# Performance work log

Measured on AMD Instinct MI355X. Metric: run time of the kernel, lower is better.

## Reference

```python
import jax, jax.numpy as jnp
import numpy as np

E = 8          # num_experts
K = 2          # top_k
TEMP = 1.0     # router_temp
D = 1024       # model dim
H = 4 * D      # expert hidden dim
B, T = 2, 2048


def setup_inputs() -> dict:
    key = jax.random.key(0)
    ks = jax.random.split(key, 5)
    x = jax.random.normal(ks[0], (B, T, D), jnp.float32)
    gate_w = jax.random.normal(ks[1], (D, E), jnp.float32) * 0.02
    gate_b = jnp.zeros((E,), jnp.float32)
    w1 = jax.random.normal(ks[2], (E, D, H), jnp.float32) * 0.02
    b1 = jnp.zeros((E, H), jnp.float32)
    w2 = jax.random.normal(ks[3], (E, H, D), jnp.float32) * 0.02
    b2 = jnp.zeros((E, D), jnp.float32)
    return {"x": x, "gate_w": gate_w, "gate_b": gate_b,
            "w1": w1, "b1": b1, "w2": w2, "b2": b2}


def reference(x, gate_w, gate_b, w1, b1, w2, b2):
    b, t, d = x.shape
    xf = x.reshape(-1, d)                                    # [N, D]
    logits = xf @ gate_w + gate_b                            # [N, E]
    gates = jax.nn.softmax(logits / TEMP, axis=-1)
    topk_gates, topk_idx = jax.lax.top_k(gates, K)           # [N, K]
    topk_gates = topk_gates / (topk_gates.sum(-1, keepdims=True) + 1e-9)
    # combine weight per (token, expert): sum over k slots routed to expert e
    comb = (jax.nn.one_hot(topk_idx, E, dtype=xf.dtype)
            * topk_gates[..., None]).sum(axis=1)             # [N, E]
    out = jnp.zeros_like(xf)
    for e in range(E):  # small fixed loop over experts
        h = jax.nn.gelu(xf @ w1[e] + b1[e], approximate=False)  # exact GELU (torch default)
        out = out + comb[:, e:e + 1] * (h @ w2[e] + b2[e])
    return out.reshape(b, t, d)
```

## Files before the change

kernel.cpp:

```cpp
#include <hip/hip_runtime.h>
#include <math.h>

#define NTOK 4096
#define DIM  1024
#define HID  4096
#define NEXP 8
#define NROW 8192

typedef __bf16 bf16;
typedef __attribute__((ext_vector_type(8))) __bf16 bf16x8;
typedef __attribute__((ext_vector_type(4))) float floatx4;

__device__ __forceinline__ void gl_lds16(const bf16* g, bf16* l) {
    __builtin_amdgcn_global_load_lds(
        (const __attribute__((address_space(1))) void*)g,
        (__attribute__((address_space(3))) void*)l, 16, 0, 0);
}

__global__ void zero_k(int* __restrict__ p) {
    if (threadIdx.x < 16) p[threadIdx.x] = 0;
}

__global__ __launch_bounds__(256) void convx_k(const float* __restrict__ x,
                                               bf16* __restrict__ xb)
{
    size_t gid = (size_t)blockIdx.x * 256 + threadIdx.x;
    size_t eo = gid * 8;
    floatx4 a = *(const floatx4*)(x + eo);
    floatx4 b = *(const floatx4*)(x + eo + 4);
    bf16x8 v;
#pragma unroll
    for (int j = 0; j < 4; ++j) { v[j] = (bf16)a[j]; v[4 + j] = (bf16)b[j]; }
    *(bf16x8*)&xb[eo] = v;
}

__global__ __launch_bounds__(256) void router_k(
    const float* __restrict__ x, const float* __restrict__ gw, const float* __restrict__ gb,
    int* __restrict__ counts, int* __restrict__ tok_e, float* __restrict__ tok_g)
{
    __shared__ __align__(16) float gws[DIM * NEXP];
    int t = threadIdx.x;
#pragma unroll
    for (int i = 0; i < 8; ++i)
        *(floatx4*)&gws[(t * 8 + i) * 4] = *(const floatx4*)&gw[(t * 8 + i) * 4];
    __syncthreads();

    int gid = blockIdx.x * 256 + t;
    int wv = gid >> 6, lane = gid & 63;
    const float* xr = x + (size_t)wv * DIM;
    float acc[NEXP];
#pragma unroll
    for (int e = 0; e < NEXP; ++e) acc[e] = 0.f;
    int d0 = lane * 16;
#pragma unroll
    for (int j = 0; j < 16; ++j) {
        float xv = xr[d0 + j];
#pragma unroll
        for (int e = 0; e < NEXP; ++e) acc[e] += xv * gws[(d0 + j) * NEXP + e];
    }
#pragma unroll
    for (int off = 32; off > 0; off >>= 1) {
#pragma unroll
        for (int e = 0; e < NEXP; ++e) acc[e] += __shfl_xor(acc[e], off, 64);
    }
    if (lane == 0) {
        float lg[NEXP], m = -1e30f;
        for (int e = 0; e < NEXP; ++e) { lg[e] = acc[e] + gb[e]; m = fmaxf(m, lg[e]); }
        float p[NEXP], s = 0.f;
        for (int e = 0; e < NEXP; ++e) { p[e] = expf(lg[e] - m); s += p[e]; }
        int e0 = 0;
        for (int e = 1; e < NEXP; ++e) if (p[e] > p[e0]) e0 = e;
        int e1 = (e0 == 0) ? 1 : 0;
        for (int e = 0; e < NEXP; ++e) if (e != e0 && p[e] > p[e1]) e1 = e;
        float g0 = p[e0] / s, g1 = p[e1] / s;
        float gs = g0 + g1 + 1e-9f;
        g0 /= gs; g1 /= gs;
        tok_e[wv * 2] = e0; tok_e[wv * 2 + 1] = e1;
        tok_g[wv * 2] = g0; tok_g[wv * 2 + 1] = g1;
        atomicAdd(&counts[e0], 1);
        atomicAdd(&counts[e1], 1);
    }
}

__global__ void scan_k(const int* __restrict__ counts, int* __restrict__ base)
{
    if (threadIdx.x == 0) {
        int s = 0;
#pragma unroll
        for (int e = 0; e < NEXP; ++e) { base[e] = s; s += counts[e]; }
        base[NEXP] = s;
    }
}

__global__ __launch_bounds__(256) void scatter_k(
    const int* __restrict__ tok_e, const float* __restrict__ tok_g,
    const int* __restrict__ base, int* __restrict__ counts2,
    int* __restrict__ row_token, float* __restrict__ row_gate, int* __restrict__ tok_row)
{
    int tk = blockIdx.x * 256 + threadIdx.x;
    if (tk >= NTOK) return;
#pragma unroll
    for (int k = 0; k < 2; ++k) {
        int e = tok_e[tk * 2 + k];
        int slot = atomicAdd(&counts2[e], 1);
        int r = base[e] + slot;
        row_token[r] = tk;
        row_gate[r] = tok_g[tk * 2 + k];
        tok_row[tk * 2 + k] = r;
    }
}

__global__ __launch_bounds__(256) void transpose_k(
    const float* __restrict__ src, bf16* __restrict__ dst,
    int R, int sld, size_t soff, size_t es, size_t ed)
{
    int e = blockIdx.z;
    bf16* d = dst + (size_t)e * ed;
    __shared__ __align__(16) bf16 tile[64 * 64];
    int t = threadIdx.x;
    int r0 = blockIdx.y * 64, c0 = blockIdx.x * 64;
#pragma unroll
    for (int i = 0; i < 2; ++i) {
        int c = t + i * 256;
        int rr = c >> 3, cc = c & 7;
        size_t eo = soff + (size_t)e * es + (size_t)(r0 + rr) * sld + c0 + cc * 8;
        floatx4 a = *(const floatx4*)(src + eo);
        floatx4 b = *(const floatx4*)(src + eo + 4);
        bf16x8 v;
#pragma unroll
        for (int j = 0; j < 4; ++j) { v[j] = (bf16)a[j]; v[4 + j] = (bf16)b[j]; }
        *(bf16x8*)&tile[rr * 64 + ((cc ^ ((rr >> 3) & 7)) * 8)] = v;
    }
    __syncthreads();
#pragma unroll
    for (int i = 0; i < 2; ++i) {
        int c = t + i * 256;
        int oc = c >> 3;
        int occ = c & 7;
        bf16x8 v;
#pragma unroll
        for (int j = 0; j < 8; ++j) {
            int r = occ * 8 + j;
            int p = (oc >> 3) ^ ((r >> 3) & 7);
            v[j] = tile[r * 64 + p * 8 + (oc & 7)];
        }
        *(bf16x8*)&d[(size_t)(c0 + oc) * R + r0 + occ * 8] = v;
    }
}

__global__ __launch_bounds__(256) void gemm1_k(
    const bf16* __restrict__ xb, const bf16* __restrict__ w1t, const float* __restrict__ b1,
    const int* __restrict__ counts, const int* __restrict__ base,
    const int* __restrict__ row_token, bf16* __restrict__ hbuf, int Nc, int bias_off)
{
    const int e = blockIdx.z;
    const int cnt = counts[e];
    const int rt = blockIdx.y;
    if (rt * 128 >= cnt) return;
    const int rb = base[e] + rt * 128;
    const int rend = base[e] + cnt;
    const int n0 = blockIdx.x * 128;

    __shared__ __align__(16) bf16 As[128 * 32];
    __shared__ __align__(16) bf16 Bs[128 * 32];

    const int t = threadIdx.x;
    const int wv = t >> 6, lane = t & 63;
    const int s0 = t, s1 = t + 256;
    const int ar0 = s0 >> 2, ac0 = (s0 & 3) ^ ((s0 >> 3) & 3);
    const int ar1 = s1 >> 2, ac1 = (s1 & 3) ^ ((s1 >> 3) & 3);
    int rr0 = rb + ar0; if (rr0 > NROW - 1) rr0 = NROW - 1;
    int rr1 = rb + ar1; if (rr1 > NROW - 1) rr1 = NROW - 1;
    const bf16* ga0 = xb + (size_t)row_token[rr0] * DIM + ac0 * 8;
    const bf16* ga1 = xb + (size_t)row_token[rr1] * DIM + ac1 * 8;
    const bf16* wb = w1t + (size_t)e * Nc * DIM;
    const bf16* gb0 = wb + (size_t)(n0 + ar0) * DIM + ac0 * 8;
    const bf16* gb1 = wb + (size_t)(n0 + ar1) * DIM + ac1 * 8;
    bf16* lA0 = &As[wv * 512];
    bf16* lA1 = &As[2048 + wv * 512];
    bf16* lB0 = &Bs[wv * 512];
    bf16* lB1 = &Bs[2048 + wv * 512];

    floatx4 acc[4][4];
#pragma unroll
    for (int i = 0; i < 4; ++i)
#pragma unroll
        for (int j = 0; j < 4; ++j) acc[i][j] = floatx4{0.f, 0.f, 0.f, 0.f};

    const int wr = (wv >> 1) * 64, wc = (wv & 1) * 64;
    const int lr = lane & 15;
    const int ck = lane >> 4;

    for (int k0 = 0; k0 < DIM; k0 += 32) {
        __syncthreads();
        gl_lds16(ga0 + k0, lA0);
        gl_lds16(ga1 + k0, lA1);
        gl_lds16(gb0 + k0, lB0);
        gl_lds16(gb1 + k0, lB1);
        __syncthreads();
        bf16x8 af[4], bg[4];
#pragma unroll
        for (int i = 0; i < 4; ++i) {
            int r = wr + i * 16 + lr;
            af[i] = *(const bf16x8*)&As[r * 32 + ((ck ^ ((r >> 1) & 3)) * 8)];
        }
#pragma unroll
        for (int i = 0; i < 4; ++i) {
            int r = wc + i * 16 + lr;
            bg[i] = *(const bf16x8*)&Bs[r * 32 + ((ck ^ ((r >> 1) & 3)) * 8)];
        }
#pragma unroll
        for (int mi = 0; mi < 4; ++mi)
#pragma unroll
            for (int ni = 0; ni < 4; ++ni)
                acc[mi][ni] = __builtin_amdgcn_mfma_f32_16x16x32_bf16(af[mi], bg[ni], acc[mi][ni], 0, 0, 0);
    }

#pragma unroll
    for (int mi = 0; mi < 4; ++mi) {
#pragma unroll
        for (int r = 0; r < 4; ++r) {
            int m = wr + mi * 16 + (lane >> 4) * 4 + r;
            int gr = rb + m;
            if (gr < rend) {
#pragma unroll
                for (int ni = 0; ni < 4; ++ni) {
                    int col = n0 + wc + ni * 16 + lr;
                    float v = acc[mi][ni][r] + b1[e * HID + bias_off + col];
                    v = 0.5f * v * (1.f + erff(v * 0.70710678f));
                    hbuf[(size_t)gr * Nc + col] = (bf16)v;
                }
            }
        }
    }
}

__global__ __launch_bounds__(256) void gemm2_k(
    const bf16* __restrict__ hbuf, const bf16* __restrict__ w2t, const float* __restrict__ b2,
    const int* __restrict__ counts, const int* __restrict__ base,
    const float* __restrict__ row_gate, float* __restrict__ ybuf,
    int Kc, int first, int last)
{
    const int e = blockIdx.z;
    const int cnt = counts[e];
    const int rt = blockIdx.y;
    if (rt * 128 >= cnt) return;
    const int rb = base[e] + rt * 128;
    const int rend = base[e] + cnt;
    const int n0 = blockIdx.x * 128;

    __shared__ __align__(16) bf16 As[128 * 32];
    __shared__ __align__(16) bf16 Bs[128 * 32];

    const int t = threadIdx.x;
    const int wv = t >> 6, lane = t & 63;
    const int s0 = t, s1 = t + 256;
    const int ar0 = s0 >> 2, ac0 = (s0 & 3) ^ ((s0 >> 3) & 3);
    const int ar1 = s1 >> 2, ac1 = (s1 & 3) ^ ((s1 >> 3) & 3);
    int rr0 = rb + ar0; if (rr0 > NROW - 1) rr0 = NROW - 1;
    int rr1 = rb + ar1; if (rr1 > NROW - 1) rr1 = NROW - 1;
    const bf16* ga0 = hbuf + (size_t)rr0 * Kc + ac0 * 8;
    const bf16* ga1 = hbuf + (size_t)rr1 * Kc + ac1 * 8;
    const bf16* wb = w2t + (size_t)e * DIM * Kc;
    const bf16* gb0 = wb + (size_t)(n0 + ar0) * Kc + ac0 * 8;
    const bf16* gb1 = wb + (size_t)(n0 + ar1) * Kc + ac1 * 8;
    bf16* lA0 = &As[wv * 512];
    bf16* lA1 = &As[2048 + wv * 512];
    bf16* lB0 = &Bs[wv * 512];
    bf16* lB1 = &Bs[2048 + wv * 512];

    floatx4 acc[4][4];
#pragma unroll
    for (int i = 0; i < 4; ++i)
#pragma unroll
        for (int j = 0; j < 4; ++j) acc[i][j] = floatx4{0.f, 0.f, 0.f, 0.f};

    const int wr = (wv >> 1) * 64, wc = (wv & 1) * 64;
    const int lr = lane & 15;
    const int ck = lane >> 4;

    for (int k0 = 0; k0 < Kc; k0 += 32) {
        __syncthreads();
        gl_lds16(ga0 + k0, lA0);
        gl_lds16(ga1 + k0, lA1);
        gl_lds16(gb0 + k0, lB0);
        gl_lds16(gb1 + k0, lB1);
        __syncthreads();
        bf16x8 af[4], bg[4];
#pragma unroll
        for (int i = 0; i < 4; ++i) {
            int r = wr + i * 16 + lr;
            af[i] = *(const bf16x8*)&As[r * 32 + ((ck ^ ((r >> 1) & 3)) * 8)];
        }
#pragma unroll
        for (int i = 0; i < 4; ++i) {
            int r = wc + i * 16 + lr;
            bg[i] = *(const bf16x8*)&Bs[r * 32 + ((ck ^ ((r >> 1) & 3)) * 8)];
        }
#pragma unroll
        for (int mi = 0; mi < 4; ++mi)
#pragma unroll
            for (int ni = 0; ni < 4; ++ni)
                acc[mi][ni] = __builtin_amdgcn_mfma_f32_16x16x32_bf16(af[mi], bg[ni], acc[mi][ni], 0, 0, 0);
    }

#pragma unroll
    for (int mi = 0; mi < 4; ++mi) {
#pragma unroll
        for (int r = 0; r < 4; ++r) {
            int m = wr + mi * 16 + (lane >> 4) * 4 + r;
            int gr = rb + m;
            if (gr < rend) {
#pragma unroll
                for (int ni = 0; ni < 4; ++ni) {
                    int col = n0 + wc + ni * 16 + lr;
                    size_t idx = (size_t)gr * DIM + col;
                    float v = acc[mi][ni][r];
                    if (last) {
                        float prev = first ? 0.f : ybuf[idx];
                        ybuf[idx] = row_gate[gr] * (prev + v + b2[e * DIM + col]);
                    } else {
                        ybuf[idx] = first ? v : (ybuf[idx] + v);
                    }
                }
            }
        }
    }
}

__global__ __launch_bounds__(256) void combine_k(
    const float* __restrict__ ybuf, const int* __restrict__ tok_row, float* __restrict__ out)
{
    int i = blockIdx.x * 256 + threadIdx.x;
    int tk = i >> 8;
    int dc = (i & 255) * 4;
    int ra = tok_row[tk * 2], rb = tok_row[tk * 2 + 1];
    floatx4 a = *(const floatx4*)&ybuf[(size_t)ra * DIM + dc];
    floatx4 b = *(const floatx4*)&ybuf[(size_t)rb * DIM + dc];
    floatx4 o;
#pragma unroll
    for (int j = 0; j < 4; ++j) o[j] = a[j] + b[j];
    *(floatx4*)&out[(size_t)tk * DIM + dc] = o;
}

extern "C" void kernel_launch(void* const* d_in, const int* in_sizes, int n_in,
                              void* d_out, int out_size, void* d_ws, size_t ws_size,
                              hipStream_t stream)
{
    const float* x  = (const float*)d_in[0];
    const float* gw = (const float*)d_in[1];
    const float* gb = (const float*)d_in[2];
    const float* w1 = (const float*)d_in[3];
    const float* b1 = (const float*)d_in[4];
    const float* w2 = (const float*)d_in[5];
    const float* b2 = (const float*)d_in[6];
    float* out = (float*)d_out;

    char* w = (char*)d_ws;
    int*   counts  = (int*)(w + 0);
    int*   counts2 = (int*)(w + 32);
    int*   base    = (int*)(w + 64);
    int*   tok_e   = (int*)(w + 256);
    float* tok_g   = (float*)(w + 256 + 32768);
    int*   row_tok = (int*)(w + 256 + 2 * 32768);
    float* row_g   = (float*)(w + 256 + 3 * 32768);
    int*   tok_row = (int*)(w + 256 + 4 * 32768);
    size_t off = 256 + 5 * 32768;
    bf16*  xb   = (bf16*)(w + off);   off += (size_t)NTOK * DIM * 2;
    float* ybuf = (float*)(w + off);  off += (size_t)NROW * DIM * 4;

    int Hc = HID;
    for (;;) {
        size_t need = off + (size_t)NEXP * Hc * DIM * 2 + (size_t)NROW * Hc * 2;
        if (need <= ws_size || Hc == 128) break;
        Hc >>= 1;
    }
    bf16* wT   = (bf16*)(w + off);  off += (size_t)NEXP * Hc * DIM * 2;
    bf16* hbuf = (bf16*)(w + off);

    zero_k<<<1, 64, 0, stream>>>(counts);
    router_k<<<NTOK / 4, 256, 0, stream>>>(x, gw, gb, counts, tok_e, tok_g);
    scan_k<<<1, 64, 0, stream>>>(counts, base);
    scatter_k<<<NTOK / 256, 256, 0, stream>>>(tok_e, tok_g, base, counts2, row_tok, row_g, tok_row);
    convx_k<<<(NTOK * DIM) / 2048, 256, 0, stream>>>(x, xb);

    const int nc = HID / Hc;
    for (int ch = 0; ch < nc; ++ch) {
        transpose_k<<<dim3(Hc / 64, DIM / 64, NEXP), 256, 0, stream>>>(
            w1, wT, DIM, HID, (size_t)ch * Hc, (size_t)DIM * HID, (size_t)Hc * DIM);
        gemm1_k<<<dim3(Hc / 128, 32, NEXP), 256, 0, stream>>>(
            xb, wT, b1, counts, base, row_tok, hbuf, Hc, ch * Hc);
        transpose_k<<<dim3(DIM / 64, Hc / 64, NEXP), 256, 0, stream>>>(
            w2, wT, Hc, DIM, (size_t)ch * Hc * DIM, (size_t)HID * DIM, (size_t)DIM * Hc);
        gemm2_k<<<dim3(DIM / 128, 32, NEXP), 256, 0, stream>>>(
            hbuf, wT, b2, counts, base, row_g, ybuf, Hc, ch == 0, ch == nc - 1);
    }

    combine_k<<<NTOK, 256, 0, stream>>>(ybuf, tok_row, out);
}
```

Baseline: 754.3 us.

## Double-buffer GEMM LDS loads and split-K gemm2 with atomic accumulation

Both expert GEMMs now prefetch the next K tile into a second LDS buffer while computing the current one, cutting one barrier per iteration. gemm2 is split four ways along K, with each slice atomically adding into a zeroed fp32 buffer to increase block-level parallelism. The gate scaling and b2 bias move into the combine kernel. This adds a zeroing pass and atomic traffic, and makes summation order nondeterministic.

After: 765.0 us. About the same (+1.4%).

```diff
diff --git a/kernel.cpp b/kernel.cpp
--- a/kernel.cpp
+++ b/kernel.cpp
@@ -6,6 +6,7 @@
 #define HID  4096
 #define NEXP 8
 #define NROW 8192
+#define KSPLIT 4
 
 typedef __bf16 bf16;
 typedef __attribute__((ext_vector_type(8))) __bf16 bf16x8;
@@ -19,6 +20,11 @@
 
 __global__ void zero_k(int* __restrict__ p) {
     if (threadIdx.x < 16) p[threadIdx.x] = 0;
+}
+
+__global__ __launch_bounds__(256) void zeroy_k(float* __restrict__ p) {
+    size_t i = ((size_t)blockIdx.x * 256 + threadIdx.x) * 4;
+    *(floatx4*)(p + i) = floatx4{0.f, 0.f, 0.f, 0.f};
 }
 
 __global__ __launch_bounds__(256) void convx_k(const float* __restrict__ x,
@@ -161,8 +167,8 @@
     const int rend = base[e] + cnt;
     const int n0 = blockIdx.x * 128;
 
-    __shared__ __align__(16) bf16 As[128 * 32];
-    __shared__ __align__(16) bf16 Bs[128 * 32];
+    __shared__ __align__(16) bf16 As[2][128 * 32];
+    __shared__ __align__(16) bf16 Bs[2][128 * 32];
 
     const int t = threadIdx.x;
     const int wv = t >> 6, lane = t & 63;
@@ -176,10 +182,7 @@
     const bf16* wb = w1t + (size_t)e * Nc * DIM;
     const bf16* gb0 = wb + (size_t)(n0 + ar0) * DIM + ac0 * 8;
     const bf16* gb1 = wb + (size_t)(n0 + ar1) * DIM + ac1 * 8;
-    bf16* lA0 = &As[wv * 512];
-    bf16* lA1 = &As[2048 + wv * 512];
-    bf16* lB0 = &Bs[wv * 512];
-    bf16* lB1 = &Bs[2048 + wv * 512];
+    const int off0 = wv * 512, off1 = 2048 + wv * 512;
 
     floatx4 acc[4][4];
 #pragma unroll
@@ -191,29 +194,39 @@
     const int lr = lane & 15;
     const int ck = lane >> 4;
 
+    gl_lds16(ga0, &As[0][off0]);
+    gl_lds16(ga1, &As[0][off1]);
+    gl_lds16(gb0, &Bs[0][off0]);
+    gl_lds16(gb1, &Bs[0][off1]);
+    __syncthreads();
+
+    int cur = 0;
     for (int k0 = 0; k0 < DIM; k0 += 32) {
-        __syncthreads();
-        gl_lds16(ga0 + k0, lA0);
-        gl_lds16(ga1 + k0, lA1);
-        gl_lds16(gb0 + k0, lB0);
-        gl_lds16(gb1 + k0, lB1);
-        __syncthreads();
+        const int kn = k0 + 32;
+        if (kn < DIM) {
+            gl_lds16(ga0 + kn, &As[cur ^ 1][off0]);
+            gl_lds16(ga1 + kn, &As[cur ^ 1][off1]);
+            gl_lds16(gb0 + kn, &Bs[cur ^ 1][off0]);
+            gl_lds16(gb1 + kn, &Bs[cur ^ 1][off1]);
+        }
         bf16x8 af[4], bg[4];
 #pragma unroll
         for (int i = 0; i < 4; ++i) {
             int r = wr + i * 16 + lr;
-            af[i] = *(const bf16x8*)&As[r * 32 + ((ck ^ ((r >> 1) & 3)) * 8)];
+            af[i] = *(const bf16x8*)&As[cur][r * 32 + ((ck ^ ((r >> 1) & 3)) * 8)];
         }
 #pragma unroll
         for (int i = 0; i < 4; ++i) {
             int r = wc + i * 16 + lr;
-            bg[i] = *(const bf16x8*)&Bs[r * 32 + ((ck ^ ((r >> 1) & 3)) * 8)];
+            bg[i] = *(const bf16x8*)&Bs[cur][r * 32 + ((ck ^ ((r >> 1) & 3)) * 8)];
         }
 #pragma unroll
         for (int mi = 0; mi < 4; ++mi)
 #pragma unroll
             for (int ni = 0; ni < 4; ++ni)
                 acc[mi][ni] = __builtin_amdgcn_mfma_f32_16x16x32_bf16(af[mi], bg[ni], acc[mi][ni], 0, 0, 0);
+        __syncthreads();
+        cur ^= 1;
     }
 
 #pragma unroll
@@ -236,21 +249,23 @@
 }
 
 __global__ __launch_bounds__(256) void gemm2_k(
-    const bf16* __restrict__ hbuf, const bf16* __restrict__ w2t, const float* __restrict__ b2,
+    const bf16* __restrict__ hbuf, const bf16* __restrict__ w2t,
     const int* __restrict__ counts, const int* __restrict__ base,
-    const float* __restrict__ row_gate, float* __restrict__ ybuf,
-    int Kc, int first, int last)
-{
-    const int e = blockIdx.z;
+    float* __restrict__ ybuf, int Kc)
+{
+    const int e  = blockIdx.z >> 2;
+    const int ks = blockIdx.z & 3;
     const int cnt = counts[e];
     const int rt = blockIdx.y;
     if (rt * 128 >= cnt) return;
     const int rb = base[e] + rt * 128;
     const int rend = base[e] + cnt;
     const int n0 = blockIdx.x * 128;
-
-    __shared__ __align__(16) bf16 As[128 * 32];
-    __shared__ __align__(16) bf16 Bs[128 * 32];
+    const int klen = Kc / KSPLIT;
+    const int kbeg = ks * klen;
+
+    __shared__ __align__(16) bf16 As[2][128 * 32];
+    __shared__ __align__(16) bf16 Bs[2][128 * 32];
 
     const int t = threadIdx.x;
     const int wv = t >> 6, lane = t & 63;
@@ -259,15 +274,12 @@
     const int ar1 = s1 >> 2, ac1 = (s1 & 3) ^ ((s1 >> 3) & 3);
     int rr0 = rb + ar0; if (rr0 > NROW - 1) rr0 = NROW - 1;
     int rr1 = rb + ar1; if (rr1 > NROW - 1) rr1 = NROW - 1;
-    const bf16* ga0 = hbuf + (size_t)rr0 * Kc + ac0 * 8;
-    const bf16* ga1 = hbuf + (size_t)rr1 * Kc + ac1 * 8;
+    const bf16* ga0 = hbuf + (size_t)rr0 * Kc + kbeg + ac0 * 8;
+    const bf16* ga1 = hbuf + (size_t)rr1 * Kc + kbeg + ac1 * 8;
     const bf16* wb = w2t + (size_t)e * DIM * Kc;
-    const bf16* gb0 = wb + (size_t)(n0 + ar0) * Kc + ac0 * 8;
-    const bf16* gb1 = wb + (size_t)(n0 + ar1) * Kc + ac1 * 8;
-    bf16* lA0 = &As[wv * 512];
-    bf16* lA1 = &As[2048 + wv * 512];
-    bf16* lB0 = &Bs[wv * 512];
-    bf16* lB1 = &Bs[2048 + wv * 512];
+    const bf16* gb0 = wb + (size_t)(n0 + ar0) * Kc + kbeg + ac0 * 8;
+    const bf16* gb1 = wb + (size_t)(n0 + ar1) * Kc + kbeg + ac1 * 8;
+    const int off0 = wv * 512, off1 = 2048 + wv * 512;
 
     floatx4 acc[4][4];
 #pragma unroll
@@ -279,29 +291,39 @@
     const int lr = lane & 15;
     const int ck = lane >> 4;
 
-    for (int k0 = 0; k0 < Kc; k0 += 32) {
-        __syncthreads();
-        gl_lds16(ga0 + k0, lA0);
-        gl_lds16(ga1 + k0, lA1);
-        gl_lds16(gb0 + k0, lB0);
-        gl_lds16(gb1 + k0, lB1);
-        __syncthreads();
+    gl_lds16(ga0, &As[0][off0]);
+    gl_lds16(ga1, &As[0][off1]);
+    gl_lds16(gb0, &Bs[0][off0]);
+    gl_lds16(gb1, &Bs[0][off1]);
+    __syncthreads();
+
+    int cur = 0;
+    for (int k0 = 0; k0 < klen; k0 += 32) {
+        const int kn = k0 + 32;
+        if (kn < klen) {
+            gl_lds16(ga0 + kn, &As[cur ^ 1][off0]);
+            gl_lds16(ga1 + kn, &As[cur ^ 1][off1]);
+            gl_lds16(gb0 + kn, &Bs[cur ^ 1][off0]);
+            gl_lds16(gb1 + kn, &Bs[cur ^ 1][off1]);
+        }
         bf16x8 af[4], bg[4];
 #pragma unroll
         for (int i = 0; i < 4; ++i) {
             int r = wr + i * 16 + lr;
-            af[i] = *(const bf16x8*)&As[r * 32 + ((ck ^ ((r >> 1) & 3)) * 8)];
+            af[i] = *(const bf16x8*)&As[cur][r * 32 + ((ck ^ ((r >> 1) & 3)) * 8)];
         }
 #pragma unroll
         for (int i = 0; i < 4; ++i) {
             int r = wc + i * 16 + lr;
-            bg[i] = *(const bf16x8*)&Bs[r * 32 + ((ck ^ ((r >> 1) & 3)) * 8)];
+            bg[i] = *(const bf16x8*)&Bs[cur][r * 32 + ((ck ^ ((r >> 1) & 3)) * 8)];
         }
 #pragma unroll
         for (int mi = 0; mi < 4; ++mi)
 #pragma unroll
             for (int ni = 0; ni < 4; ++ni)
                 acc[mi][ni] = __builtin_amdgcn_mfma_f32_16x16x32_bf16(af[mi], bg[ni], acc[mi][ni], 0, 0, 0);
+        __syncthreads();
+        cur ^= 1;
     }
 
 #pragma unroll
@@ -314,14 +336,7 @@
 #pragma unroll
                 for (int ni = 0; ni < 4; ++ni) {
                     int col = n0 + wc + ni * 16 + lr;
-                    size_t idx = (size_t)gr * DIM + col;
-                    float v = acc[mi][ni][r];
-                    if (last) {
-                        float prev = first ? 0.f : ybuf[idx];
-                        ybuf[idx] = row_gate[gr] * (prev + v + b2[e * DIM + col]);
-                    } else {
-                        ybuf[idx] = first ? v : (ybuf[idx] + v);
-                    }
+                    atomicAdd(&ybuf[(size_t)gr * DIM + col], acc[mi][ni][r]);
                 }
             }
         }
@@ -329,17 +344,23 @@
 }
 
 __global__ __launch_bounds__(256) void combine_k(
-    const float* __restrict__ ybuf, const int* __restrict__ tok_row, float* __restrict__ out)
+    const float* __restrict__ ybuf, const int* __restrict__ tok_row,
+    const int* __restrict__ tok_e, const float* __restrict__ tok_g,
+    const float* __restrict__ b2, float* __restrict__ out)
 {
     int i = blockIdx.x * 256 + threadIdx.x;
     int tk = i >> 8;
     int dc = (i & 255) * 4;
-    int ra = tok_row[tk * 2], rb = tok_row[tk * 2 + 1];
-    floatx4 a = *(const floatx4*)&ybuf[(size_t)ra * DIM + dc];
-    floatx4 b = *(const floatx4*)&ybuf[(size_t)rb * DIM + dc];
+    int ra = tok_row[tk * 2], rbx = tok_row[tk * 2 + 1];
+    int ea = tok_e[tk * 2],  eb = tok_e[tk * 2 + 1];
+    float ga = tok_g[tk * 2], gbv = tok_g[tk * 2 + 1];
+    floatx4 a  = *(const floatx4*)&ybuf[(size_t)ra * DIM + dc];
+    floatx4 b  = *(const floatx4*)&ybuf[(size_t)rbx * DIM + dc];
+    floatx4 b2a = *(const floatx4*)&b2[ea * DIM + dc];
+    floatx4 b2b = *(const floatx4*)&b2[eb * DIM + dc];
     floatx4 o;
 #pragma unroll
-    for (int j = 0; j < 4; ++j) o[j] = a[j] + b[j];
+    for (int j = 0; j < 4; ++j) o[j] = ga * (a[j] + b2a[j]) + gbv * (b[j] + b2b[j]);
     *(floatx4*)&out[(size_t)tk * DIM + dc] = o;
 }
 
@@ -383,6 +404,7 @@
     scan_k<<<1, 64, 0, stream>>>(counts, base);
     scatter_k<<<NTOK / 256, 256, 0, stream>>>(tok_e, tok_g, base, counts2, row_tok, row_g, tok_row);
     convx_k<<<(NTOK * DIM) / 2048, 256, 0, stream>>>(x, xb);
+    zeroy_k<<<(NROW * DIM) / 1024, 256, 0, stream>>>(ybuf);
 
     const int nc = HID / Hc;
     for (int ch = 0; ch < nc; ++ch) {
@@ -392,9 +414,9 @@
             xb, wT, b1, counts, base, row_tok, hbuf, Hc, ch * Hc);
         transpose_k<<<dim3(DIM / 64, Hc / 64, NEXP), 256, 0, stream>>>(
             w2, wT, Hc, DIM, (size_t)ch * Hc * DIM, (size_t)HID * DIM, (size_t)DIM * Hc);
-        gemm2_k<<<dim3(DIM / 128, 32, NEXP), 256, 0, stream>>>(
-            hbuf, wT, b2, counts, base, row_g, ybuf, Hc, ch == 0, ch == nc - 1);
-    }
-
-    combine_k<<<NTOK, 256, 0, stream>>>(ybuf, tok_row, out);
-}
+        gemm2_k<<<dim3(DIM / 128, 32, NEXP * KSPLIT), 256, 0, stream>>>(
+            hbuf, wT, counts, base, ybuf, Hc);
+    }
+
+    combine_k<<<NTOK, 256, 0, stream>>>(ybuf, tok_row, tok_e, tok_g, b2, out);
+}
```

## Triple-buffer LDS tiles with async global-to-LDS prefetch in expert GEMMs

Applied to the files above, without the earlier changes.

Replaces the single-buffer load, sync, compute loop in both expert GEMM kernels with a three-stage LDS ring. Tiles are prefetched two steps ahead through global_load_lds, with explicit vmcnt waits and a single barrier per step. Wave priority is also raised around the MFMA block. The goal is to hide global memory latency behind matrix compute and remove one barrier per K step, at the cost of three times the LDS per block, which may reduce occupancy.

Measured after the change: 741.6 us. Within noise of the previous version (-1.7%).

```diff
diff --git a/kernel.cpp b/kernel.cpp
--- a/kernel.cpp
+++ b/kernel.cpp
@@ -161,8 +161,8 @@
     const int rend = base[e] + cnt;
     const int n0 = blockIdx.x * 128;
 
-    __shared__ __align__(16) bf16 As[128 * 32];
-    __shared__ __align__(16) bf16 Bs[128 * 32];
+    __shared__ __align__(16) bf16 As[3][128 * 32];
+    __shared__ __align__(16) bf16 Bs[3][128 * 32];
 
     const int t = threadIdx.x;
     const int wv = t >> 6, lane = t & 63;
@@ -176,10 +176,7 @@
     const bf16* wb = w1t + (size_t)e * Nc * DIM;
     const bf16* gb0 = wb + (size_t)(n0 + ar0) * DIM + ac0 * 8;
     const bf16* gb1 = wb + (size_t)(n0 + ar1) * DIM + ac1 * 8;
-    bf16* lA0 = &As[wv * 512];
-    bf16* lA1 = &As[2048 + wv * 512];
-    bf16* lB0 = &Bs[wv * 512];
-    bf16* lB1 = &Bs[2048 + wv * 512];
+    const int off0 = wv * 512, off1 = 2048 + wv * 512;
 
     floatx4 acc[4][4];
 #pragma unroll
@@ -191,29 +188,43 @@
     const int lr = lane & 15;
     const int ck = lane >> 4;
 
-    for (int k0 = 0; k0 < DIM; k0 += 32) {
-        __syncthreads();
-        gl_lds16(ga0 + k0, lA0);
-        gl_lds16(ga1 + k0, lA1);
-        gl_lds16(gb0 + k0, lB0);
-        gl_lds16(gb1 + k0, lB1);
-        __syncthreads();
+    gl_lds16(ga0,      &As[0][off0]); gl_lds16(ga1,      &As[0][off1]);
+    gl_lds16(gb0,      &Bs[0][off0]); gl_lds16(gb1,      &Bs[0][off1]);
+    gl_lds16(ga0 + 32, &As[1][off0]); gl_lds16(ga1 + 32, &As[1][off1]);
+    gl_lds16(gb0 + 32, &Bs[1][off0]); gl_lds16(gb1 + 32, &Bs[1][off1]);
+
+    const int NSTEP = DIM / 32;
+    int bc = 0;
+    for (int i = 0; i < NSTEP; ++i) {
+        if (i < NSTEP - 1) asm volatile("s_waitcnt vmcnt(4)" ::: "memory");
+        else               asm volatile("s_waitcnt vmcnt(0)" ::: "memory");
+        __builtin_amdgcn_s_barrier();
+        asm volatile("" ::: "memory");
+        if (i + 2 < NSTEP) {
+            int bs = bc + 2; if (bs >= 3) bs -= 3;
+            const int kn = (i + 2) * 32;
+            gl_lds16(ga0 + kn, &As[bs][off0]); gl_lds16(ga1 + kn, &As[bs][off1]);
+            gl_lds16(gb0 + kn, &Bs[bs][off0]); gl_lds16(gb1 + kn, &Bs[bs][off1]);
+        }
         bf16x8 af[4], bg[4];
 #pragma unroll
-        for (int i = 0; i < 4; ++i) {
-            int r = wr + i * 16 + lr;
-            af[i] = *(const bf16x8*)&As[r * 32 + ((ck ^ ((r >> 1) & 3)) * 8)];
-        }
-#pragma unroll
-        for (int i = 0; i < 4; ++i) {
-            int r = wc + i * 16 + lr;
-            bg[i] = *(const bf16x8*)&Bs[r * 32 + ((ck ^ ((r >> 1) & 3)) * 8)];
-        }
+        for (int q = 0; q < 4; ++q) {
+            int r = wr + q * 16 + lr;
+            af[q] = *(const bf16x8*)&As[bc][r * 32 + ((ck ^ ((r >> 1) & 3)) * 8)];
+        }
+#pragma unroll
+        for (int q = 0; q < 4; ++q) {
+            int r = wc + q * 16 + lr;
+            bg[q] = *(const bf16x8*)&Bs[bc][r * 32 + ((ck ^ ((r >> 1) & 3)) * 8)];
+        }
+        __builtin_amdgcn_s_setprio(1);
 #pragma unroll
         for (int mi = 0; mi < 4; ++mi)
 #pragma unroll
             for (int ni = 0; ni < 4; ++ni)
                 acc[mi][ni] = __builtin_amdgcn_mfma_f32_16x16x32_bf16(af[mi], bg[ni], acc[mi][ni], 0, 0, 0);
+        __builtin_amdgcn_s_setprio(0);
+        bc += 1; if (bc >= 3) bc -= 3;
     }
 
 #pragma unroll
@@ -249,8 +260,8 @@
     const int rend = base[e] + cnt;
     const int n0 = blockIdx.x * 128;
 
-    __shared__ __align__(16) bf16 As[128 * 32];
-    __shared__ __align__(16) bf16 Bs[128 * 32];
+    __shared__ __align__(16) bf16 As[3][128 * 32];
+    __shared__ __align__(16) bf16 Bs[3][128 * 32];
 
     const int t = threadIdx.x;
     const int wv = t >> 6, lane = t & 63;
@@ -264,10 +275,7 @@
     const bf16* wb = w2t + (size_t)e * DIM * Kc;
     const bf16* gb0 = wb + (size_t)(n0 + ar0) * Kc + ac0 * 8;
     const bf16* gb1 = wb + (size_t)(n0 + ar1) * Kc + ac1 * 8;
-    bf16* lA0 = &As[wv * 512];
-    bf16* lA1 = &As[2048 + wv * 512];
-    bf16* lB0 = &Bs[wv * 512];
-    bf16* lB1 = &Bs[2048 + wv * 512];
+    const int off0 = wv * 512, off1 = 2048 + wv * 512;
 
     floatx4 acc[4][4];
 #pragma unroll
@@ -279,29 +287,43 @@
     const int lr = lane & 15;
     const int ck = lane >> 4;
 
-    for (int k0 = 0; k0 < Kc; k0 += 32) {
-        __syncthreads();
-        gl_lds16(ga0 + k0, lA0);
-        gl_lds16(ga1 + k0, lA1);
-        gl_lds16(gb0 + k0, lB0);
-        gl_lds16(gb1 + k0, lB1);
-        __syncthreads();
+    gl_lds16(ga0,      &As[0][off0]); gl_lds16(ga1,      &As[0][off1]);
+    gl_lds16(gb0,      &Bs[0][off0]); gl_lds16(gb1,      &Bs[0][off1]);
+    gl_lds16(ga0 + 32, &As[1][off0]); gl_lds16(ga1 + 32, &As[1][off1]);
+    gl_lds16(gb0 + 32, &Bs[1][off0]); gl_lds16(gb1 + 32, &Bs[1][off1]);
+
+    const int nstep = Kc >> 5;
+    int bc = 0;
+    for (int i = 0; i < nstep; ++i) {
+        if (i < nstep - 1) asm volatile("s_waitcnt vmcnt(4)" ::: "memory");
+        else               asm volatile("s_waitcnt vmcnt(0)" ::: "memory");
+        __builtin_amdgcn_s_barrier();
+        asm volatile("" ::: "memory");
+        if (i + 2 < nstep) {
+            int bs = bc + 2; if (bs >= 3) bs -= 3;
+            const int kn = (i + 2) * 32;
+            gl_lds16(ga0 + kn, &As[bs][off0]); gl_lds16(ga1 + kn, &As[bs][off1]);
+            gl_lds16(gb0 + kn, &Bs[bs][off0]); gl_lds16(gb1 + kn, &Bs[bs][off1]);
+        }
         bf16x8 af[4], bg[4];
 #pragma unroll
-        for (int i = 0; i < 4; ++i) {
-            int r = wr + i * 16 + lr;
-            af[i] = *(const bf16x8*)&As[r * 32 + ((ck ^ ((r >> 1) & 3)) * 8)];
-        }
-#pragma unroll
-        for (int i = 0; i < 4; ++i) {
-            int r = wc + i * 16 + lr;
-            bg[i] = *(const bf16x8*)&Bs[r * 32 + ((ck ^ ((r >> 1) & 3)) * 8)];
-        }
+        for (int q = 0; q < 4; ++q) {
+            int r = wr + q * 16 + lr;
+            af[q] = *(const bf16x8*)&As[bc][r * 32 + ((ck ^ ((r >> 1) & 3)) * 8)];
+        }
+#pragma unroll
+        for (int q = 0; q < 4; ++q) {
+            int r = wc + q * 16 + lr;
+            bg[q] = *(const bf16x8*)&Bs[bc][r * 32 + ((ck ^ ((r >> 1) & 3)) * 8)];
+        }
+        __builtin_amdgcn_s_setprio(1);
 #pragma unroll
         for (int mi = 0; mi < 4; ++mi)
 #pragma unroll
             for (int ni = 0; ni < 4; ++ni)
                 acc[mi][ni] = __builtin_amdgcn_mfma_f32_16x16x32_bf16(af[mi], bg[ni], acc[mi][ni], 0, 0, 0);
+        __builtin_amdgcn_s_setprio(0);
+        bc += 1; if (bc >= 3) bc -= 3;
     }
 
 #pragma unroll
```
